# Performance work log

Measured on AMD Instinct MI355X. Metric: run time of the kernel, lower is better.

## Reference

```python
import jax, jax.numpy as jnp
import numpy as np
from functools import partial

B, T_OUT, T_IN, L, D_IN, D_ATT = 8, 256, 512, 128, 128, 128


def setup_inputs() -> dict:
    key = jax.random.key(0)
    ks = jax.random.split(key, 8)
    s = 0.05  # small init scale for numerical stability
    return {
        "inputs": jax.random.normal(ks[0], (B, T_OUT, D_IN), jnp.float32),
        "attended_inputs": jax.random.normal(ks[1], (B, T_IN, D_ATT), jnp.float32),
        "lstm_kernel": jax.random.normal(ks[2], (D_IN, 4 * L), jnp.float32) * s,
        "lstm_rec_kernel": jax.random.normal(ks[3], (L, 4 * L), jnp.float32) * s,
        "lstm_bias": jnp.zeros((4 * L,), jnp.float32),
        "W1": jax.random.normal(ks[4], (D_ATT, L), jnp.float32) * s,
        "b1": jnp.zeros((L,), jnp.float32),
        "W2": jax.random.normal(ks[5], (L, L), jnp.float32) * s,
        "b2": jnp.zeros((L,), jnp.float32),
        "W3": jax.random.normal(ks[6], (L, 1), jnp.float32) * s,
        "b3": jnp.zeros((1,), jnp.float32),
    }


def _lstm(x, Wk, Wr, b):
    # x: (B, T, D_in). Keras gate order: i, f, c(g), o. Zero initial state.
    Bq = x.shape[0]
    h0 = jnp.zeros((Bq, L), x.dtype)
    c0 = jnp.zeros((Bq, L), x.dtype)
    xz = jnp.einsum('btd,dk->btk', x, Wk) + b  # precompute input projection

    def step(carry, zt):
        h, c = carry
        z = zt + h @ Wr
        i, f, g, o = jnp.split(z, 4, axis=-1)
        c_new = jax.nn.sigmoid(f) * c + jax.nn.sigmoid(i) * jnp.tanh(g)
        h_new = jax.nn.sigmoid(o) * jnp.tanh(c_new)
        return (h_new, c_new), h_new

    (h_T, c_T), hs = jax.lax.scan(step, (h0, c0), jnp.swapaxes(xz, 0, 1))
    return jnp.swapaxes(hs, 0, 1), h_T, c_T  # (B, T, L), (B, L), (B, L)


def reference(inputs, attended_inputs, lstm_kernel, lstm_rec_kernel, lstm_bias,
              W1, b1, W2, b2, W3, b3):
    # setup_attended: keys = dense1(attended_inputs)
    keys = attended_inputs @ W1 + b1  # (B, T_in, L)
    x, h, c = _lstm(inputs, lstm_kernel, lstm_rec_kernel, lstm_bias)  # (B, T_out, L)
    q = x @ W2 + b2  # (B, T_out, L)
    # Bahdanau additive score: tanh(keys[:,None] + q[:,:,None]) . W3 -> (B, T_out, T_in)
    t = jnp.tanh(keys[:, None, :, :] + q[:, :, None, :])  # (B, T_out, T_in, L)
    scores = jnp.einsum('bqkl,l->bqk', t, W3[:, 0]) + b3[0]
    attn = jax.nn.softmax(scores, axis=-1)
    weighted = jnp.einsum('bqk,bkd->bqd', attn, attended_inputs)  # (B, T_out, D_att)
    out = jnp.concatenate([x, weighted], axis=2)  # (B, T_out, L + D_att)
    return out, h, c
```

## Files before the change

kernel.cpp:

```cpp
#include <hip/hip_runtime.h>
#include <hip/hip_bf16.h>

#define XZ_OFF   1048576
#define KEYS_OFF 2097152
#define X_OFF    2621440
#define OUT_H    524288
#define OUT_C    525312

#define LDS_BARRIER() __asm__ __volatile__("s_waitcnt lgkmcnt(0)\n\ts_barrier" ::: "memory")

typedef _Float16 f16x8 __attribute__((ext_vector_type(8)));
typedef float fx4 __attribute__((ext_vector_type(4)));

__device__ __forceinline__ float fast_rcp(float x) { return __builtin_amdgcn_rcpf(x); }
__device__ __forceinline__ float fast_sig(float v) { return fast_rcp(1.f + __expf(-v)); }
__device__ __forceinline__ float fast_tanh(float v) { return 2.f * fast_rcp(1.f + __expf(-2.f * v)) - 1.f; }

__global__ __launch_bounds__(256)
void prologue_k(const float* __restrict__ inp, const float* __restrict__ att,
                const float* __restrict__ Wk, const float* __restrict__ bias,
                const float* __restrict__ W1, const float* __restrict__ b1,
                float* __restrict__ ws) {
  __shared__ float ar[16][128];
  const int tid = threadIdx.x;
  if (blockIdx.x < 256) {
    float* keys = ws + KEYS_OFF;
    const int row0 = blockIdx.x * 16;
    for (int i = tid; i < 16 * 128; i += 256) ar[i >> 7][i & 127] = att[row0 * 128 + i];
    __syncthreads();
    const int l = tid & 127, r0 = tid >> 7;
    float acc[8];
    const float bl = b1[l];
#pragma unroll
    for (int i = 0; i < 8; ++i) acc[i] = bl;
    for (int d = 0; d < 128; d += 4) {
      float w0 = W1[(d + 0) * 128 + l], w1 = W1[(d + 1) * 128 + l];
      float w2 = W1[(d + 2) * 128 + l], w3 = W1[(d + 3) * 128 + l];
#pragma unroll
      for (int i = 0; i < 8; ++i) {
        float4 a4 = *(const float4*)&ar[r0 + 2 * i][d];
        acc[i] += a4.x * w0 + a4.y * w1 + a4.z * w2 + a4.w * w3;
      }
    }
#pragma unroll
    for (int i = 0; i < 8; ++i) keys[(row0 + r0 + 2 * i) * 128 + l] = acc[i];
  } else {
    _Float16* xz16 = (_Float16*)(ws + XZ_OFF);
    const int row0 = (blockIdx.x - 256) * 8;
    for (int i = tid; i < 8 * 128; i += 256) ar[i >> 7][i & 127] = inp[row0 * 128 + i];
    __syncthreads();
    float acc[8][2];
    const float bb0 = bias[tid], bb1 = bias[tid + 256];
#pragma unroll
    for (int r = 0; r < 8; ++r) { acc[r][0] = bb0; acc[r][1] = bb1; }
    for (int d = 0; d < 128; d += 4) {
      float w0a = Wk[(d + 0) * 512 + tid], w0b = Wk[(d + 0) * 512 + tid + 256];
      float w1a = Wk[(d + 1) * 512 + tid], w1b = Wk[(d + 1) * 512 + tid + 256];
      float w2a = Wk[(d + 2) * 512 + tid], w2b = Wk[(d + 2) * 512 + tid + 256];
      float w3a = Wk[(d + 3) * 512 + tid], w3b = Wk[(d + 3) * 512 + tid + 256];
#pragma unroll
      for (int r = 0; r < 8; ++r) {
        float4 a4 = *(const float4*)&ar[r][d];
        acc[r][0] += a4.x * w0a + a4.y * w1a + a4.z * w2a + a4.w * w3a;
        acc[r][1] += a4.x * w0b + a4.y * w1b + a4.z * w2b + a4.w * w3b;
      }
    }
    const int u = tid & 127, g0 = tid >> 7;
#pragma unroll
    for (int r = 0; r < 8; ++r) {
      const int row = row0 + r, b = row >> 8, t = row & 255;
      const int base = ((t * 8 + b) * 128 + u) * 4;
      xz16[base + g0]     = (_Float16)acc[r][0];
      xz16[base + g0 + 2] = (_Float16)acc[r][1];
    }
  }
}

__global__ __launch_bounds__(512, 1)
void lstm_scan(const float* __restrict__ Wrf, const float* __restrict__ ws,
               float* __restrict__ out) {
  const _Float16* xz16 = (const _Float16*)(ws + XZ_OFF);
  _Float16* x16 = (_Float16*)((float*)ws + X_OFF);
  const int b_base = blockIdx.x * 4;
  const int tid = threadIdx.x;
  const int w = tid >> 6, lane = tid & 63;
  const int q = lane >> 4, p = lane & 15;
  const int b = p & 3, r = p >> 2;
  const int u = 16 * w + 4 * q + r;
  const int bg = b_base + b;

  __shared__ _Float16 hb[2][552];

  f16x8 afr[4][4];
#pragma unroll
  for (int c = 0; c < 4; ++c)
#pragma unroll
    for (int kt = 0; kt < 4; ++kt)
#pragma unroll
      for (int j = 0; j < 8; ++j)
        afr[c][kt][j] = (_Float16)Wrf[(kt * 32 + q * 8 + j) * 512 + 128 * c + 16 * w + p];

  {
    _Float16* hp = &hb[0][0];
    for (int i = tid; i < 2 * 552; i += 512) hp[i] = (_Float16)0.f;
  }
  float cst = 0.f, hval = 0.f;
  const _Float16* xp = xz16 + (bg * 128 + u) * 4;
  uint2 pf0 = *(const uint2*)(xp);
  uint2 pf1 = *(const uint2*)(xp + 4096);
  uint2 pf2 = *(const uint2*)(xp + 8192);
  __syncthreads();

  const int brow = (p & 3) * 136;
  for (int t = 0; t < 256; ++t) {
    const _Float16* hrow = &hb[t & 1][brow];
    f16x8 bfr[4];
#pragma unroll
    for (int kt = 0; kt < 4; ++kt)
      bfr[kt] = *(const f16x8*)&hrow[kt * 32 + q * 8];
    fx4 acc[4];
#pragma unroll
    for (int c = 0; c < 4; ++c) acc[c] = (fx4)0.f;
#pragma unroll
    for (int kt = 0; kt < 4; ++kt)
#pragma unroll
      for (int c = 0; c < 4; ++c)
        acc[c] = __builtin_amdgcn_mfma_f32_16x16x32_f16(afr[c][kt], bfr[kt], acc[c], 0, 0, 0);

    float z[4];
#pragma unroll
    for (int c = 0; c < 4; ++c) {
      float d1 = __int_as_float(__builtin_amdgcn_mov_dpp(__float_as_int(acc[c][1]), 0x114, 0xF, 0xF, true));
      float d2 = __int_as_float(__builtin_amdgcn_mov_dpp(__float_as_int(acc[c][2]), 0x118, 0xF, 0xF, true));
      float d3 = __int_as_float(__builtin_amdgcn_mov_dpp(__float_as_int(acc[c][3]), 0x11C, 0xF, 0xF, true));
      z[c] = (r == 0) ? acc[c][0] : (r == 1) ? d1 : (r == 2) ? d2 : d3;
    }

    uint2 cur = pf0;
    pf0 = pf1; pf1 = pf2;
    const int t3 = (t + 3 < 256) ? t + 3 : 255;
    pf2 = *(const uint2*)(xp + t3 * 4096);

    const _Float16* cf = (const _Float16*)&cur;
    const float zi = z[0] + (float)cf[0];
    const float zf = z[1] + (float)cf[1];
    const float zg = z[2] + (float)cf[2];
    const float zo = z[3] + (float)cf[3];
    cst = fast_sig(zf) * cst + fast_sig(zi) * fast_tanh(zg);
    hval = fast_sig(zo) * fast_tanh(cst);
    hb[(t + 1) & 1][b * 136 + u] = (_Float16)hval;
    x16[(bg * 256 + t) * 128 + u] = (_Float16)hval;
    LDS_BARRIER();
  }
  out[OUT_H + bg * 128 + u] = hval;
  out[OUT_C + bg * 128 + u] = cst;
}

__global__ __launch_bounds__(256)
void attn_out_k(const float* __restrict__ att, const float* __restrict__ W2c,
                const float* __restrict__ b2c, const float* __restrict__ W3c,
                const float* __restrict__ b3c, const float* __restrict__ ws,
                float* __restrict__ out) {
  const float* keys = ws + KEYS_OFF;
  const _Float16* x16 = (const _Float16*)(ws + X_OFF);
  __shared__ float qp[8][128];
  __shared__ float xr[8][128];
  __shared__ float sc[8][512];
  __shared__ float kt[64][129];
  __shared__ float w3s[128];
  const int tid = threadIdx.x;
  const int b = blockIdx.x >> 5, qt = blockIdx.x & 31;
  const int q0 = qt * 8;
  const int l = tid & 127, r0 = tid >> 7;
  if (tid < 128) w3s[tid] = W3c[tid];
  for (int i = tid; i < 8 * 128; i += 256)
    xr[i >> 7][i & 127] = (float)x16[(b * 256 + q0) * 128 + i];
  __syncthreads();
  {
    float qa[4];
    const float bl = b2c[l];
#pragma unroll
    for (int i = 0; i < 4; ++i) qa[i] = bl;
    for (int d = 0; d < 128; d += 4) {
      float w0 = W2c[(d + 0) * 128 + l], w1 = W2c[(d + 1) * 128 + l];
      float w2v = W2c[(d + 2) * 128 + l], w3v = W2c[(d + 3) * 128 + l];
#pragma unroll
      for (int i = 0; i < 4; ++i) {
        float4 a4 = *(const float4*)&xr[r0 + 2 * i][d];
        qa[i] += a4.x * w0 + a4.y * w1 + a4.z * w2v + a4.w * w3v;
      }
    }
#pragma unroll
    for (int i = 0; i < 4; ++i) {
      int rr = r0 + 2 * i;
      qp[rr][l] = qa[i];
      out[(b * 256 + q0 + rr) * 256 + l] = xr[rr][l];
    }
  }
  const float b3v = b3c[0];
  for (int kt0 = 0; kt0 < 512; kt0 += 64) {
    __syncthreads();
    for (int i = tid; i < 64 * 128; i += 256)
      kt[i >> 7][i & 127] = keys[(b * 512 + kt0 + (i >> 7)) * 128 + (i & 127)];
    __syncthreads();
#pragma unroll
    for (int pp = 0; pp < 2; ++pp) {
      const int pidx = tid + pp * 256;
      const int rr = pidx >> 6, k = pidx & 63;
      float acc = 0.f;
      for (int ll = 0; ll < 128; ll += 4) {
        float4 q4 = *(const float4*)&qp[rr][ll];
        float4 w4 = *(const float4*)&w3s[ll];
        acc += fast_tanh(kt[k][ll + 0] + q4.x) * w4.x
             + fast_tanh(kt[k][ll + 1] + q4.y) * w4.y
             + fast_tanh(kt[k][ll + 2] + q4.z) * w4.z
             + fast_tanh(kt[k][ll + 3] + q4.w) * w4.w;
      }
      sc[rr][kt0 + k] = acc + b3v;
    }
  }
  __syncthreads();
  {
    const int wave = tid >> 6, lane = tid & 63;
    for (int rr = wave; rr < 8; rr += 4) {
      float v[8];
#pragma unroll
      for (int i = 0; i < 8; ++i) v[i] = sc[rr][lane + i * 64];
      float m = v[0];
#pragma unroll
      for (int i = 1; i < 8; ++i) m = fmaxf(m, v[i]);
#pragma unroll
      for (int off = 32; off > 0; off >>= 1) m = fmaxf(m, __shfl_xor(m, off));
      float e[8], s = 0.f;
#pragma unroll
      for (int i = 0; i < 8; ++i) { e[i] = __expf(v[i] - m); s += e[i]; }
#pragma unroll
      for (int off = 32; off > 0; off >>= 1) s += __shfl_xor(s, off);
      const float inv = fast_rcp(s);
#pragma unroll
      for (int i = 0; i < 8; ++i) sc[rr][lane + i * 64] = e[i] * inv;
    }
  }
  __syncthreads();
  {
    const float* attb = att + b * 512 * 128;
    float wa[4] = {0.f, 0.f, 0.f, 0.f};
    for (int k = 0; k < 512; k += 4) {
      float a0 = attb[(k + 0) * 128 + l];
      float a1 = attb[(k + 1) * 128 + l];
      float a2 = attb[(k + 2) * 128 + l];
      float a3 = attb[(k + 3) * 128 + l];
#pragma unroll
      for (int i = 0; i < 4; ++i) {
        float4 p4 = *(const float4*)&sc[r0 + 2 * i][k];
        wa[i] += p4.x * a0 + p4.y * a1 + p4.z * a2 + p4.w * a3;
      }
    }
#pragma unroll
    for (int i = 0; i < 4; ++i)
      out[(b * 256 + q0 + r0 + 2 * i) * 256 + 128 + l] = wa[i];
  }
}

extern "C" void kernel_launch(void* const* d_in, const int* in_sizes, int n_in,
                              void* d_out, int out_size, void* d_ws, size_t ws_size,
                              hipStream_t stream) {
  const float* inputs   = (const float*)d_in[0];
  const float* attended = (const float*)d_in[1];
  const float* Wk       = (const float*)d_in[2];
  const float* Wr       = (const float*)d_in[3];
  const float* bias     = (const float*)d_in[4];
  const float* W1       = (const float*)d_in[5];
  const float* b1       = (const float*)d_in[6];
  const float* W2       = (const float*)d_in[7];
  const float* b2       = (const float*)d_in[8];
  const float* W3       = (const float*)d_in[9];
  const float* b3       = (const float*)d_in[10];
  float* out = (float*)d_out;
  float* ws = (float*)d_ws;

  hipLaunchKernelGGL(prologue_k, dim3(512), dim3(256), 0, stream,
                     inputs, attended, Wk, bias, W1, b1, ws);
  hipLaunchKernelGGL(lstm_scan, dim3(2), dim3(512), 0, stream, Wr, ws, out);
  hipLaunchKernelGGL(attn_out_k, dim3(256), dim3(256), 0, stream,
                     attended, W2, b2, W3, b3, ws, out);
}
```

Baseline: 318.3 us.

## Overlap keys projection with LSTM scan and remap MFMA gate layout

The keys projection moves out of the prologue and into extra blocks of the scan launch, so it runs alongside the two serial LSTM blocks instead of ahead of them. The recurrent weight fragments are permuted so that each lane gets its four gate values by register selects rather than DPP cross-lane moves. The first MFMA now takes a zero accumulator, which drops the explicit clear. The attention kernel is also split into blocks of 4 query rows instead of 8, doubling the grid for more parallelism, at the cost of reloading the keys more often per query.

Result: faster. 307.7 us (-3.3%).

```diff
diff --git a/kernel.cpp b/kernel.cpp
--- a/kernel.cpp
+++ b/kernel.cpp
@@ -17,93 +17,97 @@
 __device__ __forceinline__ float fast_tanh(float v) { return 2.f * fast_rcp(1.f + __expf(-2.f * v)) - 1.f; }
 
 __global__ __launch_bounds__(256)
-void prologue_k(const float* __restrict__ inp, const float* __restrict__ att,
-                const float* __restrict__ Wk, const float* __restrict__ bias,
-                const float* __restrict__ W1, const float* __restrict__ b1,
-                float* __restrict__ ws) {
+void xz_prologue(const float* __restrict__ inp, const float* __restrict__ Wk,
+                 const float* __restrict__ bias, float* __restrict__ ws) {
+  _Float16* xz16 = (_Float16*)(ws + XZ_OFF);
+  __shared__ float ar[8][128];
+  const int tid = threadIdx.x;
+  const int row0 = blockIdx.x * 8;
+  for (int i = tid; i < 8 * 128; i += 256) ar[i >> 7][i & 127] = inp[row0 * 128 + i];
+  __syncthreads();
+  float acc[8][2];
+  const float bb0 = bias[tid], bb1 = bias[tid + 256];
+#pragma unroll
+  for (int r = 0; r < 8; ++r) { acc[r][0] = bb0; acc[r][1] = bb1; }
+  for (int d = 0; d < 128; d += 4) {
+    float w0a = Wk[(d + 0) * 512 + tid], w0b = Wk[(d + 0) * 512 + tid + 256];
+    float w1a = Wk[(d + 1) * 512 + tid], w1b = Wk[(d + 1) * 512 + tid + 256];
+    float w2a = Wk[(d + 2) * 512 + tid], w2b = Wk[(d + 2) * 512 + tid + 256];
+    float w3a = Wk[(d + 3) * 512 + tid], w3b = Wk[(d + 3) * 512 + tid + 256];
+#pragma unroll
+    for (int r = 0; r < 8; ++r) {
+      float4 a4 = *(const float4*)&ar[r][d];
+      acc[r][0] += a4.x * w0a + a4.y * w1a + a4.z * w2a + a4.w * w3a;
+      acc[r][1] += a4.x * w0b + a4.y * w1b + a4.z * w2b + a4.w * w3b;
+    }
+  }
+  const int u = tid & 127, g0 = tid >> 7;
+#pragma unroll
+  for (int r = 0; r < 8; ++r) {
+    const int row = row0 + r, b = row >> 8, t = row & 255;
+    const int base = ((t * 8 + b) * 128 + u) * 4;
+    xz16[base + g0]     = (_Float16)acc[r][0];
+    xz16[base + g0 + 2] = (_Float16)acc[r][1];
+  }
+}
+
+__global__ __launch_bounds__(512, 1)
+void lstm_scan(const float* __restrict__ Wrf, const float* __restrict__ att,
+               const float* __restrict__ W1, const float* __restrict__ b1,
+               const float* __restrict__ ws, float* __restrict__ out) {
+  __shared__ _Float16 hb[2][552];
   __shared__ float ar[16][128];
   const int tid = threadIdx.x;
-  if (blockIdx.x < 256) {
-    float* keys = ws + KEYS_OFF;
-    const int row0 = blockIdx.x * 16;
-    for (int i = tid; i < 16 * 128; i += 256) ar[i >> 7][i & 127] = att[row0 * 128 + i];
+
+  if (blockIdx.x >= 2) {
+    float* keys = (float*)ws + KEYS_OFF;
+    const int row0 = (blockIdx.x - 2) * 16;
+    for (int i = tid; i < 16 * 128; i += 512) ar[i >> 7][i & 127] = att[row0 * 128 + i];
     __syncthreads();
     const int l = tid & 127, r0 = tid >> 7;
-    float acc[8];
+    float acc[4];
     const float bl = b1[l];
 #pragma unroll
-    for (int i = 0; i < 8; ++i) acc[i] = bl;
+    for (int i = 0; i < 4; ++i) acc[i] = bl;
     for (int d = 0; d < 128; d += 4) {
       float w0 = W1[(d + 0) * 128 + l], w1 = W1[(d + 1) * 128 + l];
       float w2 = W1[(d + 2) * 128 + l], w3 = W1[(d + 3) * 128 + l];
 #pragma unroll
-      for (int i = 0; i < 8; ++i) {
-        float4 a4 = *(const float4*)&ar[r0 + 2 * i][d];
+      for (int i = 0; i < 4; ++i) {
+        float4 a4 = *(const float4*)&ar[r0 + 4 * i][d];
         acc[i] += a4.x * w0 + a4.y * w1 + a4.z * w2 + a4.w * w3;
       }
     }
 #pragma unroll
-    for (int i = 0; i < 8; ++i) keys[(row0 + r0 + 2 * i) * 128 + l] = acc[i];
-  } else {
-    _Float16* xz16 = (_Float16*)(ws + XZ_OFF);
-    const int row0 = (blockIdx.x - 256) * 8;
-    for (int i = tid; i < 8 * 128; i += 256) ar[i >> 7][i & 127] = inp[row0 * 128 + i];
-    __syncthreads();
-    float acc[8][2];
-    const float bb0 = bias[tid], bb1 = bias[tid + 256];
-#pragma unroll
-    for (int r = 0; r < 8; ++r) { acc[r][0] = bb0; acc[r][1] = bb1; }
-    for (int d = 0; d < 128; d += 4) {
-      float w0a = Wk[(d + 0) * 512 + tid], w0b = Wk[(d + 0) * 512 + tid + 256];
-      float w1a = Wk[(d + 1) * 512 + tid], w1b = Wk[(d + 1) * 512 + tid + 256];
-      float w2a = Wk[(d + 2) * 512 + tid], w2b = Wk[(d + 2) * 512 + tid + 256];
-      float w3a = Wk[(d + 3) * 512 + tid], w3b = Wk[(d + 3) * 512 + tid + 256];
-#pragma unroll
-      for (int r = 0; r < 8; ++r) {
-        float4 a4 = *(const float4*)&ar[r][d];
-        acc[r][0] += a4.x * w0a + a4.y * w1a + a4.z * w2a + a4.w * w3a;
-        acc[r][1] += a4.x * w0b + a4.y * w1b + a4.z * w2b + a4.w * w3b;
-      }
-    }
-    const int u = tid & 127, g0 = tid >> 7;
-#pragma unroll
-    for (int r = 0; r < 8; ++r) {
-      const int row = row0 + r, b = row >> 8, t = row & 255;
-      const int base = ((t * 8 + b) * 128 + u) * 4;
-      xz16[base + g0]     = (_Float16)acc[r][0];
-      xz16[base + g0 + 2] = (_Float16)acc[r][1];
-    }
-  }
-}
-
-__global__ __launch_bounds__(512, 1)
-void lstm_scan(const float* __restrict__ Wrf, const float* __restrict__ ws,
-               float* __restrict__ out) {
+    for (int i = 0; i < 4; ++i) keys[(row0 + r0 + 4 * i) * 128 + l] = acc[i];
+    return;
+  }
+
   const _Float16* xz16 = (const _Float16*)(ws + XZ_OFF);
   _Float16* x16 = (_Float16*)((float*)ws + X_OFF);
   const int b_base = blockIdx.x * 4;
-  const int tid = threadIdx.x;
   const int w = tid >> 6, lane = tid & 63;
   const int q = lane >> 4, p = lane & 15;
-  const int b = p & 3, r = p >> 2;
-  const int u = 16 * w + 4 * q + r;
+  const int b = p & 3, isel = p >> 2;
+  const int u = 16 * w + 4 * isel + q;
   const int bg = b_base + b;
 
-  __shared__ _Float16 hb[2][552];
-
   f16x8 afr[4][4];
 #pragma unroll
-  for (int c = 0; c < 4; ++c)
+  for (int i = 0; i < 4; ++i) {
+    const int col = (p & 3) * 128 + 16 * w + 4 * i + (p >> 2);
 #pragma unroll
     for (int kt = 0; kt < 4; ++kt)
 #pragma unroll
       for (int j = 0; j < 8; ++j)
-        afr[c][kt][j] = (_Float16)Wrf[(kt * 32 + q * 8 + j) * 512 + 128 * c + 16 * w + p];
+        afr[i][kt][j] = (_Float16)Wrf[(kt * 32 + q * 8 + j) * 512 + col];
+  }
 
   {
     _Float16* hp = &hb[0][0];
     for (int i = tid; i < 2 * 552; i += 512) hp[i] = (_Float16)0.f;
   }
+  const fx4 zeroC = {0.f, 0.f, 0.f, 0.f};
   float cst = 0.f, hval = 0.f;
   const _Float16* xp = xz16 + (bg * 128 + u) * 4;
   uint2 pf0 = *(const uint2*)(xp);
@@ -120,20 +124,20 @@
       bfr[kt] = *(const f16x8*)&hrow[kt * 32 + q * 8];
     fx4 acc[4];
 #pragma unroll
-    for (int c = 0; c < 4; ++c) acc[c] = (fx4)0.f;
-#pragma unroll
-    for (int kt = 0; kt < 4; ++kt)
-#pragma unroll
-      for (int c = 0; c < 4; ++c)
-        acc[c] = __builtin_amdgcn_mfma_f32_16x16x32_f16(afr[c][kt], bfr[kt], acc[c], 0, 0, 0);
+    for (int i = 0; i < 4; ++i)
+      acc[i] = __builtin_amdgcn_mfma_f32_16x16x32_f16(afr[i][0], bfr[0], zeroC, 0, 0, 0);
+#pragma unroll
+    for (int kt = 1; kt < 4; ++kt)
+#pragma unroll
+      for (int i = 0; i < 4; ++i)
+        acc[i] = __builtin_amdgcn_mfma_f32_16x16x32_f16(afr[i][kt], bfr[kt], acc[i], 0, 0, 0);
 
     float z[4];
 #pragma unroll
-    for (int c = 0; c < 4; ++c) {
-      float d1 = __int_as_float(__builtin_amdgcn_mov_dpp(__float_as_int(acc[c][1]), 0x114, 0xF, 0xF, true));
-      float d2 = __int_as_float(__builtin_amdgcn_mov_dpp(__float_as_int(acc[c][2]), 0x118, 0xF, 0xF, true));
-      float d3 = __int_as_float(__builtin_amdgcn_mov_dpp(__float_as_int(acc[c][3]), 0x11C, 0xF, 0xF, true));
-      z[c] = (r == 0) ? acc[c][0] : (r == 1) ? d1 : (r == 2) ? d2 : d3;
+    for (int r = 0; r < 4; ++r) {
+      float s01 = (isel & 1) ? acc[1][r] : acc[0][r];
+      float s23 = (isel & 1) ? acc[3][r] : acc[2][r];
+      z[r] = (isel & 2) ? s23 : s01;
     }
 
     uint2 cur = pf0;
@@ -163,35 +167,33 @@
                 float* __restrict__ out) {
   const float* keys = ws + KEYS_OFF;
   const _Float16* x16 = (const _Float16*)(ws + X_OFF);
-  __shared__ float qp[8][128];
-  __shared__ float xr[8][128];
-  __shared__ float sc[8][512];
+  __shared__ float qp[4][128];
+  __shared__ float xr[4][128];
+  __shared__ float sc[4][512];
   __shared__ float kt[64][129];
   __shared__ float w3s[128];
   const int tid = threadIdx.x;
-  const int b = blockIdx.x >> 5, qt = blockIdx.x & 31;
-  const int q0 = qt * 8;
+  const int b = blockIdx.x >> 6, q0 = (blockIdx.x & 63) * 4;
   const int l = tid & 127, r0 = tid >> 7;
   if (tid < 128) w3s[tid] = W3c[tid];
-  for (int i = tid; i < 8 * 128; i += 256)
+  for (int i = tid; i < 4 * 128; i += 256)
     xr[i >> 7][i & 127] = (float)x16[(b * 256 + q0) * 128 + i];
   __syncthreads();
   {
-    float qa[4];
+    float qa[2];
     const float bl = b2c[l];
-#pragma unroll
-    for (int i = 0; i < 4; ++i) qa[i] = bl;
+    qa[0] = bl; qa[1] = bl;
     for (int d = 0; d < 128; d += 4) {
       float w0 = W2c[(d + 0) * 128 + l], w1 = W2c[(d + 1) * 128 + l];
       float w2v = W2c[(d + 2) * 128 + l], w3v = W2c[(d + 3) * 128 + l];
 #pragma unroll
-      for (int i = 0; i < 4; ++i) {
+      for (int i = 0; i < 2; ++i) {
         float4 a4 = *(const float4*)&xr[r0 + 2 * i][d];
         qa[i] += a4.x * w0 + a4.y * w1 + a4.z * w2v + a4.w * w3v;
       }
     }
 #pragma unroll
-    for (int i = 0; i < 4; ++i) {
+    for (int i = 0; i < 2; ++i) {
       int rr = r0 + 2 * i;
       qp[rr][l] = qa[i];
       out[(b * 256 + q0 + rr) * 256 + l] = xr[rr][l];
@@ -203,10 +205,8 @@
     for (int i = tid; i < 64 * 128; i += 256)
       kt[i >> 7][i & 127] = keys[(b * 512 + kt0 + (i >> 7)) * 128 + (i & 127)];
     __syncthreads();
-#pragma unroll
-    for (int pp = 0; pp < 2; ++pp) {
-      const int pidx = tid + pp * 256;
-      const int rr = pidx >> 6, k = pidx & 63;
+    {
+      const int rr = tid >> 6, k = tid & 63;
       float acc = 0.f;
       for (int ll = 0; ll < 128; ll += 4) {
         float4 q4 = *(const float4*)&qp[rr][ll];
@@ -222,42 +222,40 @@
   __syncthreads();
   {
     const int wave = tid >> 6, lane = tid & 63;
-    for (int rr = wave; rr < 8; rr += 4) {
-      float v[8];
-#pragma unroll
-      for (int i = 0; i < 8; ++i) v[i] = sc[rr][lane + i * 64];
-      float m = v[0];
-#pragma unroll
-      for (int i = 1; i < 8; ++i) m = fmaxf(m, v[i]);
-#pragma unroll
-      for (int off = 32; off > 0; off >>= 1) m = fmaxf(m, __shfl_xor(m, off));
-      float e[8], s = 0.f;
-#pragma unroll
-      for (int i = 0; i < 8; ++i) { e[i] = __expf(v[i] - m); s += e[i]; }
-#pragma unroll
-      for (int off = 32; off > 0; off >>= 1) s += __shfl_xor(s, off);
-      const float inv = fast_rcp(s);
-#pragma unroll
-      for (int i = 0; i < 8; ++i) sc[rr][lane + i * 64] = e[i] * inv;
-    }
+    float v[8];
+#pragma unroll
+    for (int i = 0; i < 8; ++i) v[i] = sc[wave][lane + i * 64];
+    float m = v[0];
+#pragma unroll
+    for (int i = 1; i < 8; ++i) m = fmaxf(m, v[i]);
+#pragma unroll
+    for (int off = 32; off > 0; off >>= 1) m = fmaxf(m, __shfl_xor(m, off));
+    float e[8], s = 0.f;
+#pragma unroll
+    for (int i = 0; i < 8; ++i) { e[i] = __expf(v[i] - m); s += e[i]; }
+#pragma unroll
+    for (int off = 32; off > 0; off >>= 1) s += __shfl_xor(s, off);
+    const float inv = fast_rcp(s);
+#pragma unroll
+    for (int i = 0; i < 8; ++i) sc[wave][lane + i * 64] = e[i] * inv;
   }
   __syncthreads();
   {
     const float* attb = att + b * 512 * 128;
-    float wa[4] = {0.f, 0.f, 0.f, 0.f};
+    float wa[2] = {0.f, 0.f};
     for (int k = 0; k < 512; k += 4) {
       float a0 = attb[(k + 0) * 128 + l];
       float a1 = attb[(k + 1) * 128 + l];
       float a2 = attb[(k + 2) * 128 + l];
       float a3 = attb[(k + 3) * 128 + l];
 #pragma unroll
-      for (int i = 0; i < 4; ++i) {
+      for (int i = 0; i < 2; ++i) {
         float4 p4 = *(const float4*)&sc[r0 + 2 * i][k];
         wa[i] += p4.x * a0 + p4.y * a1 + p4.z * a2 + p4.w * a3;
       }
     }
 #pragma unroll
-    for (int i = 0; i < 4; ++i)
+    for (int i = 0; i < 2; ++i)
       out[(b * 256 + q0 + r0 + 2 * i) * 256 + 128 + l] = wa[i];
   }
 }
@@ -279,9 +277,9 @@
   float* out = (float*)d_out;
   float* ws = (float*)d_ws;
 
-  hipLaunchKernelGGL(prologue_k, dim3(512), dim3(256), 0, stream,
-                     inputs, attended, Wk, bias, W1, b1, ws);
-  hipLaunchKernelGGL(lstm_scan, dim3(2), dim3(512), 0, stream, Wr, ws, out);
-  hipLaunchKernelGGL(attn_out_k, dim3(256), dim3(256), 0, stream,
+  hipLaunchKernelGGL(xz_prologue, dim3(256), dim3(256), 0, stream, inputs, Wk, bias, ws);
+  hipLaunchKernelGGL(lstm_scan, dim3(258), dim3(512), 0, stream,
+                     Wr, attended, W1, b1, ws, out);
+  hipLaunchKernelGGL(attn_out_k, dim3(512), dim3(256), 0, stream,
                      attended, W2, b2, W3, b3, ws, out);
 }
```
